# Optimization experiments

Hardware: AMD Instinct MI355X
Metric: run time of the kernel (lower is better)

## Reference

```python
import jax, jax.numpy as jnp
import numpy as np

B = 64          # batch_size
N_PER = 1000    # num_nodes per graph
NTOT = B * N_PER
H = 64          # hidden_gnn_dim


def _gcn_aggregate(x, senders, receivers, add_self_edges):
    """jraph.GraphConvolution aggregation with symmetric normalization.
    x: [NTOT, F] node features AFTER update_node_fn."""
    if add_self_edges:
        self_idx = jnp.arange(NTOT, dtype=senders.dtype)
        s = jnp.concatenate([senders, self_idx])
        r = jnp.concatenate([receivers, self_idx])
    else:
        s, r = senders, receivers
    ones = jnp.ones_like(s, dtype=x.dtype)
    deg_s = jax.ops.segment_sum(ones, s, num_segments=NTOT)
    deg_r = jax.ops.segment_sum(ones, r, num_segments=NTOT)
    x = x * jax.lax.rsqrt(jnp.maximum(deg_s, 1.0))[:, None]
    x = jax.ops.segment_sum(x[s], r, num_segments=NTOT)
    x = x * jax.lax.rsqrt(jnp.maximum(deg_r, 1.0))[:, None]
    return x


def setup_inputs() -> dict:
    key = jax.random.key(0)
    ks = jax.random.split(key, 12)
    n_edges = 1_000_000
    in_dim, fc, lat, out_dim = 64, 512, 64, 32
    flat = N_PER * H  # 64000

    def w(k, shape, fan_in):
        return jax.random.normal(k, shape, dtype=jnp.float32) / np.sqrt(fan_in)

    return {
        "nodes": jax.random.normal(ks[0], (NTOT, in_dim), dtype=jnp.float32),
        "senders": jax.random.randint(ks[1], (n_edges,), 0, NTOT),
        "receivers": jax.random.randint(ks[2], (n_edges,), 0, NTOT),
        "eps": jax.random.normal(ks[3], (B, lat), dtype=jnp.float32),
        "W_gcn1": w(ks[4], (in_dim, H), in_dim),
        "b_gcn1": jnp.zeros((H,), jnp.float32),
        "W_fc": w(ks[5], (flat, fc), flat),
        "b_fc": jnp.zeros((fc,), jnp.float32),
        "W_mean": w(ks[6], (fc, lat), fc),
        "b_mean": jnp.zeros((lat,), jnp.float32),
        "W_logstd": w(ks[7], (fc, lat), fc),
        "b_logstd": jnp.zeros((lat,), jnp.float32),
        "W_dec_fc": w(ks[8], (lat, flat), lat),
        "b_dec_fc": jnp.zeros((flat,), jnp.float32),
        "W_dec_out": w(ks[9], (H, out_dim), H),
        "b_dec_out": jnp.zeros((out_dim,), jnp.float32),
    }


def reference(nodes, senders, receivers, eps, W_gcn1, b_gcn1, W_fc, b_fc,
              W_mean, b_mean, W_logstd, b_logstd, W_dec_fc, b_dec_fc,
              W_dec_out, b_dec_out):
    # --- Encoder: GCN(update=Linear+relu, add_self_edges=True) ---
    h = jax.nn.relu(nodes @ W_gcn1 + b_gcn1)                 # [NTOT, H]
    h = _gcn_aggregate(h, senders, receivers, add_self_edges=True)
    x = h.reshape(B, N_PER * H)                              # flatten per graph
    x = jax.nn.relu(x @ W_fc + b_fc)                         # [B, fc]
    mean = x @ W_mean + b_mean                               # [B, lat]
    log_std = x @ W_logstd + b_logstd                        # [B, lat]
    # --- Reparameterization ---
    z = mean + jnp.exp(log_std) * eps                        # [B, lat]
    # --- Decoder ---
    d = jax.nn.relu(z @ W_dec_fc + b_dec_fc)                 # [B, N_PER*H]
    d = d.reshape(NTOT, H)
    d = d @ W_dec_out + b_dec_out                            # update_node_fn
    out_nodes = _gcn_aggregate(d, senders, receivers, add_self_edges=False)
    return mean, log_std, out_nodes
```

## Files before the change

kernel.cpp:

```cpp
#include <hip/hip_runtime.h>
#include <math.h>

#define NTOT 64000
#define HD   64
#define NB   64
#define FC   512
#define LAT  64
#define OUTD 32
#define GKC  128
#define NKB  500
#define NBH  128
#define NBUK 250
#define BSH  8
#define BCH  3968

typedef __bf16 bf16x8 __attribute__((ext_vector_type(8)));
typedef float  f32x4  __attribute__((ext_vector_type(4)));

__device__ inline float bflo(unsigned u) { union {unsigned q; float f;} x; x.q = u << 16; return x.f; }
__device__ inline float bfhi(unsigned u) { union {unsigned q; float f;} x; x.q = u & 0xFFFF0000u; return x.f; }
__device__ inline unsigned pkbf(float lo, float hi) {
  __bf16 a = (__bf16)lo, b = (__bf16)hi;
  unsigned short ua, ub;
  __builtin_memcpy(&ua, &a, 2); __builtin_memcpy(&ub, &b, 2);
  return (unsigned)ua | ((unsigned)ub << 16);
}

__global__ __launch_bounds__(256) void k_hist(const int* __restrict__ s,
    const int* __restrict__ r, unsigned* __restrict__ partials, int nE) {
  __shared__ unsigned hist[16000];
  int arr = blockIdx.y;
  const int* idx = arr ? r : s;
  unsigned* base = partials + ((size_t)arr * NBH + blockIdx.x) * 16000;
  for (int u = threadIdx.x; u < 16000; u += 256) hist[u] = 0;
  __syncthreads();
  int chunk = (nE + NBH - 1) / NBH;
  int e0 = blockIdx.x * chunk;
  int e1 = min(e0 + chunk, nE);
  for (int e = e0 + threadIdx.x; e < e1; e += 256) {
    int i = idx[e];
    atomicAdd(&hist[i >> 2], 1u << ((i & 3) * 8));
  }
  __syncthreads();
  for (int u = threadIdx.x; u < 16000; u += 256) base[u] = hist[u];
}

__global__ __launch_bounds__(256) void k_scan1(const unsigned* __restrict__ partials,
    int* __restrict__ rs, int* __restrict__ bsums,
    int* __restrict__ dout, int* __restrict__ din) {
  __shared__ int sm[256];
  __shared__ unsigned bw[64];
  int t = threadIdx.x;
  int w0 = blockIdx.x * 64;
  if (t < 64) {
    unsigned a = 0, b = 0;
    for (int bk = 0; bk < NBH; bk++) a += partials[(size_t)bk * 16000 + w0 + t];
    for (int bk = 0; bk < NBH; bk++) b += partials[((size_t)NBH + bk) * 16000 + w0 + t];
    bw[t] = b;
    *reinterpret_cast<int4*>(dout + (size_t)(w0 + t) * 4) =
        make_int4(a & 255, (a >> 8) & 255, (a >> 16) & 255, a >> 24);
    *reinterpret_cast<int4*>(din + (size_t)(w0 + t) * 4) =
        make_int4(b & 255, (b >> 8) & 255, (b >> 16) & 255, b >> 24);
  }
  __syncthreads();
  int v = (int)((bw[t >> 2] >> ((t & 3) * 8)) & 255u);
  sm[t] = v;
  __syncthreads();
  for (int d = 1; d < 256; d <<= 1) {
    int x = (t >= d) ? sm[t - d] : 0;
    __syncthreads();
    sm[t] += x;
    __syncthreads();
  }
  rs[blockIdx.x * 256 + t] = sm[t] - v;
  if (t == 255) bsums[blockIdx.x] = sm[255];
}

__global__ void k_scan2(int* __restrict__ rs, int* __restrict__ gcur,
                        const int* __restrict__ bsums, int nE) {
  __shared__ int sm[256];
  int bid = blockIdx.x, t = threadIdx.x;
  sm[t] = (t < bid) ? bsums[t] : 0;
  __syncthreads();
  for (int d = 128; d > 0; d >>= 1) {
    if (t < d) sm[t] += sm[t + d];
    __syncthreads();
  }
  int i = bid * 256 + t;
  int v = rs[i] + sm[0];
  rs[i] = v;
  if ((i & 255) == 0) gcur[i >> 8] = v;
  if (bid == 0 && t == 0) rs[NTOT] = nE;
}

__global__ __launch_bounds__(256) void k_bucket(const int* __restrict__ s,
    const int* __restrict__ r, int* __restrict__ gcur,
    unsigned* __restrict__ ebuf, int nE) {
  __shared__ int cnt[NBUK];
  __shared__ int base[NBUK];
  __shared__ int rbuf[BCH];
  int tid = threadIdx.x;
  int chunk = (nE + gridDim.x - 1) / gridDim.x;
  int e0 = blockIdx.x * chunk;
  int e1 = min(e0 + chunk, nE);
  for (int u = tid; u < NBUK; u += 256) cnt[u] = 0;
  __syncthreads();
  for (int e = e0 + tid; e < e1; e += 256) {
    int rr = r[e];
    rbuf[e - e0] = rr;
    atomicAdd(&cnt[rr >> BSH], 1);
  }
  __syncthreads();
  for (int u = tid; u < NBUK; u += 256) {
    base[u] = atomicAdd(&gcur[u], cnt[u]);
    cnt[u] = 0;
  }
  __syncthreads();
  for (int e = e0 + tid; e < e1; e += 256) {
    int rr = rbuf[e - e0];
    int b = rr >> BSH;
    int off = atomicAdd(&cnt[b], 1);
    ebuf[base[b] + off] = ((unsigned)(rr & 255) << 16) | (unsigned)s[e];
  }
}

__global__ __launch_bounds__(256) void k_fill2(const unsigned* __restrict__ ebuf,
    const int* __restrict__ rs, int* __restrict__ csr) {
  __shared__ int cur[256];
  int b = blockIdx.x;
  int tid = threadIdx.x;
  int nbase = b << BSH;
  cur[tid] = rs[nbase + tid];
  __syncthreads();
  int e0 = rs[nbase];
  int e1 = rs[nbase + 256];
  for (int e = e0 + tid; e < e1; e += 256) {
    unsigned p = ebuf[e];
    int pos = atomicAdd(&cur[p >> 16], 1);
    csr[pos] = (int)(p & 0xFFFFu);
  }
}

__global__ __launch_bounds__(256) void k_node1(const float* __restrict__ nodes,
    const float* __restrict__ W1, const float* __restrict__ b1,
    const int* __restrict__ dout, __bf16* __restrict__ h1) {
  __shared__ float wsm[HD * HD];
  int tid = threadIdx.x;
  for (int u = tid; u < HD * HD; u += 256) wsm[u] = W1[u];
  __syncthreads();
  int f = tid & 63, g = tid >> 6;
#pragma unroll
  for (int it = 0; it < 4; it++) {
    int node = blockIdx.x * 16 + it * 4 + g;
    const float* xr = nodes + (size_t)node * HD;
    float acc = b1[f];
#pragma unroll 16
    for (int k = 0; k < HD; k++) acc = fmaf(xr[k], wsm[k * HD + f], acc);
    acc = fmaxf(acc, 0.f);
    h1[(size_t)node * HD + f] = (__bf16)(acc * rsqrtf((float)(dout[node] + 1)));
  }
}

__global__ __launch_bounds__(256) void k_agg1(const unsigned* __restrict__ h1u,
    const int* __restrict__ rs, const int* __restrict__ csr,
    const int* __restrict__ din, unsigned* __restrict__ xbo) {
  int tid = threadIdx.x;
  int node = blockIdx.x * 8 + (tid >> 5);
  int f2 = tid & 31;
  int beg = rs[node], end = rs[node + 1];
  unsigned su = h1u[(size_t)node * 32 + f2];
  float a0 = bflo(su), b0 = bfhi(su);
  float a1 = 0, b1 = 0, a2 = 0, b2 = 0, a3 = 0, b3 = 0;
  float a4 = 0, b4 = 0, a5 = 0, b5 = 0, a6 = 0, b6 = 0, a7 = 0, b7 = 0;
  int e = beg;
  for (; e + 8 <= end; e += 8) {
    unsigned u0 = h1u[(size_t)csr[e] * 32 + f2];
    unsigned u1 = h1u[(size_t)csr[e + 1] * 32 + f2];
    unsigned u2 = h1u[(size_t)csr[e + 2] * 32 + f2];
    unsigned u3 = h1u[(size_t)csr[e + 3] * 32 + f2];
    unsigned u4 = h1u[(size_t)csr[e + 4] * 32 + f2];
    unsigned u5 = h1u[(size_t)csr[e + 5] * 32 + f2];
    unsigned u6 = h1u[(size_t)csr[e + 6] * 32 + f2];
    unsigned u7 = h1u[(size_t)csr[e + 7] * 32 + f2];
    a0 += bflo(u0); b0 += bfhi(u0);
    a1 += bflo(u1); b1 += bfhi(u1);
    a2 += bflo(u2); b2 += bfhi(u2);
    a3 += bflo(u3); b3 += bfhi(u3);
    a4 += bflo(u4); b4 += bfhi(u4);
    a5 += bflo(u5); b5 += bfhi(u5);
    a6 += bflo(u6); b6 += bfhi(u6);
    a7 += bflo(u7); b7 += bfhi(u7);
  }
  for (; e + 4 <= end; e += 4) {
    unsigned u0 = h1u[(size_t)csr[e] * 32 + f2];
    unsigned u1 = h1u[(size_t)csr[e + 1] * 32 + f2];
    unsigned u2 = h1u[(size_t)csr[e + 2] * 32 + f2];
    unsigned u3 = h1u[(size_t)csr[e + 3] * 32 + f2];
    a0 += bflo(u0); b0 += bfhi(u0);
    a1 += bflo(u1); b1 += bfhi(u1);
    a2 += bflo(u2); b2 += bfhi(u2);
    a3 += bflo(u3); b3 += bfhi(u3);
  }
  for (; e < end; e++) {
    unsigned u = h1u[(size_t)csr[e] * 32 + f2];
    a1 += bflo(u); b1 += bfhi(u);
  }
  float sc = rsqrtf((float)(din[node] + 1));
  float sa = ((a0 + a1) + (a2 + a3)) + ((a4 + a5) + (a6 + a7));
  float sb = ((b0 + b1) + (b2 + b3)) + ((b4 + b5) + (b6 + b7));
  xbo[(size_t)node * 32 + f2] = pkbf(sa * sc, sb * sc);
}

__global__ __launch_bounds__(512) void k_gemm(const __bf16* __restrict__ xb,
    const float* __restrict__ Wfc, unsigned* __restrict__ part) {
  __shared__ __align__(16) __bf16 As[64 * 136];
  int kb = blockIdx.x;
  int k0 = kb * GKC;
  int tid = threadIdx.x;
  for (int u = tid; u < 64 * 16; u += 512) {
    int row = u >> 4, c = u & 15;
    const uint4* src = reinterpret_cast<const uint4*>(xb + (size_t)row * 64000 + k0);
    reinterpret_cast<uint4*>(&As[row * 136])[c] = src[c];
  }
  __syncthreads();
  int w = tid >> 6, lane = tid & 63;
  int cw = lane & 15, kg = lane >> 4;
  const float* Bp = Wfc + ((size_t)k0 + kg * 8) * FC + w * 64 + cw;
  f32x4 acc[4][4];
#pragma unroll
  for (int mt = 0; mt < 4; mt++)
#pragma unroll
    for (int nt = 0; nt < 4; nt++) acc[mt][nt] = (f32x4){0.f, 0.f, 0.f, 0.f};

  for (int ks = 0; ks < 4; ks++) {
    bf16x8 bfrag[4];
#pragma unroll
    for (int nt = 0; nt < 4; nt++) {
      const float* bp = Bp + (size_t)ks * 32 * FC + nt * 16;
      bf16x8 bb;
#pragma unroll
      for (int b = 0; b < 8; b++) bb[b] = (__bf16)bp[(size_t)b * FC];
      bfrag[nt] = bb;
    }
    bf16x8 afrag[4];
#pragma unroll
    for (int mt = 0; mt < 4; mt++)
      afrag[mt] = *reinterpret_cast<const bf16x8*>(
          &As[(mt * 16 + cw) * 136 + ks * 32 + kg * 8]);
#pragma unroll
    for (int mt = 0; mt < 4; mt++)
#pragma unroll
      for (int nt = 0; nt < 4; nt++)
        acc[mt][nt] = __builtin_amdgcn_mfma_f32_16x16x32_bf16(
            afrag[mt], bfrag[nt], acc[mt][nt], 0, 0, 0);
  }
#pragma unroll
  for (int mt = 0; mt < 4; mt++)
#pragma unroll
    for (int nt = 0; nt < 4; nt++) {
      int col = w * 64 + nt * 16 + cw;
      size_t base = (size_t)kb * (FC * 32) + (size_t)col * 32 + mt * 8 + kg * 2;
      part[base]     = pkbf(acc[mt][nt][0], acc[mt][nt][1]);
      part[base + 1] = pkbf(acc[mt][nt][2], acc[mt][nt][3]);
    }
}

__global__ __launch_bounds__(256) void k_reduce(const unsigned* __restrict__ part,
    const float* __restrict__ bfc, float* __restrict__ xf) {
  __shared__ float slo[8][33];
  __shared__ float shi[8][33];
  int t = threadIdx.x;
  int pl = t & 31, sl = t >> 5;
  int c = blockIdx.x;
  size_t off = (size_t)c * 32 + pl;
  float lo0 = 0, hi0 = 0, lo1 = 0, hi1 = 0;
  int kb = sl;
  for (; kb + 16 < NKB; kb += 16) {
    unsigned u0 = part[(size_t)kb * (FC * 32) + off];
    unsigned u1 = part[(size_t)(kb + 8) * (FC * 32) + off];
    lo0 += bflo(u0); hi0 += bfhi(u0);
    lo1 += bflo(u1); hi1 += bfhi(u1);
  }
  for (; kb < NKB; kb += 8) {
    unsigned u0 = part[(size_t)kb * (FC * 32) + off];
    lo0 += bflo(u0); hi0 += bfhi(u0);
  }
  slo[sl][pl] = lo0 + lo1;
  shi[sl][pl] = hi0 + hi1;
  __syncthreads();
  if (t < 32) {
    float lo = 0, hi = 0;
#pragma unroll
    for (int s = 0; s < 8; s++) { lo += slo[s][t]; hi += shi[s][t]; }
    float bias = bfc[c];
    xf[(size_t)(2 * t) * FC + c]     = fmaxf(lo + bias, 0.f);
    xf[(size_t)(2 * t + 1) * FC + c] = fmaxf(hi + bias, 0.f);
  }
}

__global__ __launch_bounds__(256) void k_head(const float* __restrict__ xf,
    const float* __restrict__ Wm, const float* __restrict__ bm,
    const float* __restrict__ Wl, const float* __restrict__ bl,
    const float* __restrict__ eps, float* __restrict__ out_mean,
    float* __restrict__ out_logstd, float* __restrict__ z) {
  __shared__ float xr[FC];
  __shared__ float ps[4][LAT];
  __shared__ float zm[LAT];
  int b = blockIdx.x, t = threadIdx.x;
  for (int u = t; u < FC; u += 256) xr[u] = xf[b * FC + u];
  __syncthreads();
  int g = t >> 6;
  int l = t & 63;
  int h = g & 1;
  const float* W = (g < 2) ? Wm : Wl;
  float acc = 0.f;
  int kb = h * (FC / 2);
#pragma unroll 8
  for (int k = kb; k < kb + FC / 2; k++) acc = fmaf(xr[k], W[k * LAT + l], acc);
  ps[g][l] = acc;
  __syncthreads();
  float ls = 0.f;
  if (g == 0) {
    float m = ps[0][l] + ps[1][l] + bm[l];
    out_mean[b * 64 + l] = m;
    zm[l] = m;
  }
  if (g == 2) {
    ls = ps[2][l] + ps[3][l] + bl[l];
    out_logstd[b * 64 + l] = ls;
  }
  __syncthreads();
  if (g == 2) z[b * 64 + l] = zm[l] + expf(ls) * eps[b * 64 + l];
}

__global__ __launch_bounds__(256) void k_dec(const float* __restrict__ z,
    const float* __restrict__ Wdf, const float* __restrict__ bdf,
    const float* __restrict__ Wdo, const float* __restrict__ bdo,
    const int* __restrict__ deg, __bf16* __restrict__ dds) {
  __shared__ float zs[64 * 64];
  __shared__ float ws[64 * 65];
  __shared__ float ps[64 * 65];
  __shared__ float wo[64 * 32];
  int np = blockIdx.x, tid = threadIdx.x;
  for (int u = tid; u < 4096; u += 256) zs[u] = z[u];
  for (int u = tid; u < 4096; u += 256)
    ws[(u >> 6) * 65 + (u & 63)] = Wdf[(size_t)(u >> 6) * 64000 + np * 64 + (u & 63)];
  for (int u = tid; u < 2048; u += 256) wo[u] = Wdo[u];
  __syncthreads();
  {
    int h = tid & 63, bg = tid >> 6;
    float bias = bdf[np * 64 + h];
#pragma unroll
    for (int bb = 0; bb < 16; bb++) {
      int b = bg * 16 + bb;
      float acc = bias;
#pragma unroll 8
      for (int k = 0; k < 64; k++) acc = fmaf(zs[b * 64 + k], ws[k * 65 + h], acc);
      ps[b * 65 + h] = fmaxf(acc, 0.f);
    }
  }
  __syncthreads();
  {
    int o = tid & 31, bg = tid >> 5;
    float bias = bdo[o];
#pragma unroll
    for (int bb = 0; bb < 8; bb++) {
      int b = bg * 8 + bb;
      float acc = bias;
#pragma unroll 8
      for (int h = 0; h < 64; h++) acc = fmaf(ps[b * 65 + h], wo[h * 32 + o], acc);
      int node = b * 1000 + np;
      dds[(size_t)node * OUTD + o] =
          (__bf16)(acc * rsqrtf(fmaxf((float)deg[node], 1.f)));
    }
  }
}

__global__ __launch_bounds__(256) void k_agg2(const unsigned* __restrict__ ddsu,
    const int* __restrict__ rs, const int* __restrict__ csr,
    const int* __restrict__ din, float* __restrict__ outn) {
  int tid = threadIdx.x;
  int node = blockIdx.x * 16 + (tid >> 4);
  int f2 = tid & 15;
  int beg = rs[node], end = rs[node + 1];
  float a0 = 0, b0 = 0, a1 = 0, b1 = 0, a2 = 0, b2 = 0, a3 = 0, b3 = 0;
  float a4 = 0, b4 = 0, a5 = 0, b5 = 0, a6 = 0, b6 = 0, a7 = 0, b7 = 0;
  int e = beg;
  for (; e + 8 <= end; e += 8) {
    unsigned u0 = ddsu[(size_t)csr[e] * 16 + f2];
    unsigned u1 = ddsu[(size_t)csr[e + 1] * 16 + f2];
    unsigned u2 = ddsu[(size_t)csr[e + 2] * 16 + f2];
    unsigned u3 = ddsu[(size_t)csr[e + 3] * 16 + f2];
    unsigned u4 = ddsu[(size_t)csr[e + 4] * 16 + f2];
    unsigned u5 = ddsu[(size_t)csr[e + 5] * 16 + f2];
    unsigned u6 = ddsu[(size_t)csr[e + 6] * 16 + f2];
    unsigned u7 = ddsu[(size_t)csr[e + 7] * 16 + f2];
    a0 += bflo(u0); b0 += bfhi(u0);
    a1 += bflo(u1); b1 += bfhi(u1);
    a2 += bflo(u2); b2 += bfhi(u2);
    a3 += bflo(u3); b3 += bfhi(u3);
    a4 += bflo(u4); b4 += bfhi(u4);
    a5 += bflo(u5); b5 += bfhi(u5);
    a6 += bflo(u6); b6 += bfhi(u6);
    a7 += bflo(u7); b7 += bfhi(u7);
  }
  for (; e + 4 <= end; e += 4) {
    unsigned u0 = ddsu[(size_t)csr[e] * 16 + f2];
    unsigned u1 = ddsu[(size_t)csr[e + 1] * 16 + f2];
    unsigned u2 = ddsu[(size_t)csr[e + 2] * 16 + f2];
    unsigned u3 = ddsu[(size_t)csr[e + 3] * 16 + f2];
    a0 += bflo(u0); b0 += bfhi(u0);
    a1 += bflo(u1); b1 += bfhi(u1);
    a2 += bflo(u2); b2 += bfhi(u2);
    a3 += bflo(u3); b3 += bfhi(u3);
  }
  for (; e < end; e++) {
    unsigned u = ddsu[(size_t)csr[e] * 16 + f2];
    a1 += bflo(u); b1 += bfhi(u);
  }
  float sc = rsqrtf(fmaxf((float)din[node], 1.f));
  float sa = ((a0 + a1) + (a2 + a3)) + ((a4 + a5) + (a6 + a7));
  float sb = ((b0 + b1) + (b2 + b3)) + ((b4 + b5) + (b6 + b7));
  *reinterpret_cast<float2*>(outn + (size_t)node * 32 + f2 * 2) =
      make_float2(sa * sc, sb * sc);
}

extern "C" void kernel_launch(void* const* d_in, const int* in_sizes, int n_in,
                              void* d_out, int out_size, void* d_ws, size_t ws_size,
                              hipStream_t stream) {
  const float* nodes   = (const float*)d_in[0];
  const int*   senders = (const int*)d_in[1];
  const int*   recvs   = (const int*)d_in[2];
  const float* eps     = (const float*)d_in[3];
  const float* W1      = (const float*)d_in[4];
  const float* b1      = (const float*)d_in[5];
  const float* Wfc     = (const float*)d_in[6];
  const float* bfc     = (const float*)d_in[7];
  const float* Wm      = (const float*)d_in[8];
  const float* bm      = (const float*)d_in[9];
  const float* Wl      = (const float*)d_in[10];
  const float* bl      = (const float*)d_in[11];
  const float* Wdf     = (const float*)d_in[12];
  const float* bdf     = (const float*)d_in[13];
  const float* Wdo     = (const float*)d_in[14];
  const float* bdo     = (const float*)d_in[15];
  int nE = in_sizes[1];

  char* w = (char*)d_ws;
  auto alloc = [&](size_t bytes) {
    char* p = w;
    w += (bytes + 255) & ~(size_t)255;
    return p;
  };
  int* deg_out   = (int*)alloc((size_t)NTOT * 4);
  int* deg_in    = (int*)alloc((size_t)NTOT * 4);
  int* row_start = (int*)alloc((size_t)(NTOT + 1) * 4);
  int* gcur      = (int*)alloc((size_t)NBUK * 4);
  int* bsums     = (int*)alloc(256 * 4);
  int* csr       = (int*)alloc((size_t)nE * 4);
  unsigned* ebuf = (unsigned*)alloc((size_t)nE * 4);
  __bf16* h1  = (__bf16*)alloc((size_t)NTOT * HD * 2);
  __bf16* xb  = (__bf16*)alloc((size_t)NTOT * HD * 2);
  unsigned* part = (unsigned*)alloc((size_t)NKB * FC * 32 * 4);
  float* xf   = (float*)alloc((size_t)NB * FC * 4);
  float* z    = (float*)alloc((size_t)NB * LAT * 4);
  __bf16* dds  = xb;
  unsigned* partials = (unsigned*)part;

  float* out_mean   = (float*)d_out;
  float* out_logstd = (float*)d_out + 4096;
  float* out_nodes  = (float*)d_out + 8192;

  k_hist<<<dim3(NBH, 2), 256, 0, stream>>>(senders, recvs, partials, nE);
  k_scan1<<<NTOT / 256, 256, 0, stream>>>(partials, row_start, bsums, deg_out, deg_in);
  k_scan2<<<NTOT / 256, 256, 0, stream>>>(row_start, gcur, bsums, nE);
  k_bucket<<<256, 256, 0, stream>>>(senders, recvs, gcur, ebuf, nE);
  k_fill2<<<NBUK, 256, 0, stream>>>(ebuf, row_start, csr);
  k_node1<<<NTOT / 16, 256, 0, stream>>>(nodes, W1, b1, deg_out, h1);
  k_agg1<<<NTOT / 8, 256, 0, stream>>>((const unsigned*)h1, row_start, csr, deg_in, (unsigned*)xb);
  k_gemm<<<NKB, 512, 0, stream>>>(xb, Wfc, part);
  k_reduce<<<FC, 256, 0, stream>>>(part, bfc, xf);
  k_head<<<NB, 256, 0, stream>>>(xf, Wm, bm, Wl, bl, eps, out_mean, out_logstd, z);
  k_dec<<<1000, 256, 0, stream>>>(z, Wdf, bdf, Wdo, bdo, deg_out, dds);
  k_agg2<<<NTOT / 16, 256, 0, stream>>>((const unsigned*)dds, row_start, csr, deg_in, out_nodes);
}
```

Measured before the change: 238.9 us.

## Fuse CSR fill into first aggregation, use 16-bit CSR, parallelize scan1 reduction

Drops the separate k_fill2 kernel. A new k_fagg1 kernel builds each 256-node bucket's CSR slice in shared memory, writes it out as 16-bit sender indices, and then aggregates the first GCN layer from that local copy. The second aggregation reads the 16-bit CSR, which halves its index traffic. k_scan1 now spreads the histogram reduction across all 256 threads instead of 64. The price is a much coarser launch (250 blocks of 1024 threads, 8 nodes per warp-group in sequence), which may lower occupancy and latency hiding. Any bucket with more than 6144 edges would silently drop edges.

```diff
diff --git a/kernel.cpp b/kernel.cpp
--- a/kernel.cpp
+++ b/kernel.cpp
@@ -13,6 +13,7 @@
 #define NBUK 250
 #define BSH  8
 #define BCH  3968
+#define LCSR 6144
 
 typedef __bf16 bf16x8 __attribute__((ext_vector_type(8)));
 typedef float  f32x4  __attribute__((ext_vector_type(4)));
@@ -49,13 +50,25 @@
     int* __restrict__ rs, int* __restrict__ bsums,
     int* __restrict__ dout, int* __restrict__ din) {
   __shared__ int sm[256];
+  __shared__ unsigned pa[4][64];
+  __shared__ unsigned pb[4][64];
   __shared__ unsigned bw[64];
   int t = threadIdx.x;
   int w0 = blockIdx.x * 64;
+  int wd = t & 63, q = t >> 6;
+  {
+    unsigned a = 0, b = 0;
+    for (int bk = q * 32; bk < q * 32 + 32; bk++) {
+      a += partials[(size_t)bk * 16000 + w0 + wd];
+      b += partials[((size_t)NBH + bk) * 16000 + w0 + wd];
+    }
+    pa[q][wd] = a;
+    pb[q][wd] = b;
+  }
+  __syncthreads();
   if (t < 64) {
-    unsigned a = 0, b = 0;
-    for (int bk = 0; bk < NBH; bk++) a += partials[(size_t)bk * 16000 + w0 + t];
-    for (int bk = 0; bk < NBH; bk++) b += partials[((size_t)NBH + bk) * 16000 + w0 + t];
+    unsigned a = (pa[0][t] + pa[1][t]) + (pa[2][t] + pa[3][t]);
+    unsigned b = (pb[0][t] + pb[1][t]) + (pb[2][t] + pb[3][t]);
     bw[t] = b;
     *reinterpret_cast<int4*>(dout + (size_t)(w0 + t) * 4) =
         make_int4(a & 255, (a >> 8) & 255, (a >> 16) & 255, a >> 24);
@@ -124,23 +137,6 @@
   }
 }
 
-__global__ __launch_bounds__(256) void k_fill2(const unsigned* __restrict__ ebuf,
-    const int* __restrict__ rs, int* __restrict__ csr) {
-  __shared__ int cur[256];
-  int b = blockIdx.x;
-  int tid = threadIdx.x;
-  int nbase = b << BSH;
-  cur[tid] = rs[nbase + tid];
-  __syncthreads();
-  int e0 = rs[nbase];
-  int e1 = rs[nbase + 256];
-  for (int e = e0 + tid; e < e1; e += 256) {
-    unsigned p = ebuf[e];
-    int pos = atomicAdd(&cur[p >> 16], 1);
-    csr[pos] = (int)(p & 0xFFFFu);
-  }
-}
-
 __global__ __launch_bounds__(256) void k_node1(const float* __restrict__ nodes,
     const float* __restrict__ W1, const float* __restrict__ b1,
     const int* __restrict__ dout, __bf16* __restrict__ h1) {
@@ -161,54 +157,75 @@
   }
 }
 
-__global__ __launch_bounds__(256) void k_agg1(const unsigned* __restrict__ h1u,
-    const int* __restrict__ rs, const int* __restrict__ csr,
-    const int* __restrict__ din, unsigned* __restrict__ xbo) {
-  int tid = threadIdx.x;
-  int node = blockIdx.x * 8 + (tid >> 5);
-  int f2 = tid & 31;
-  int beg = rs[node], end = rs[node + 1];
-  unsigned su = h1u[(size_t)node * 32 + f2];
-  float a0 = bflo(su), b0 = bfhi(su);
-  float a1 = 0, b1 = 0, a2 = 0, b2 = 0, a3 = 0, b3 = 0;
-  float a4 = 0, b4 = 0, a5 = 0, b5 = 0, a6 = 0, b6 = 0, a7 = 0, b7 = 0;
-  int e = beg;
-  for (; e + 8 <= end; e += 8) {
-    unsigned u0 = h1u[(size_t)csr[e] * 32 + f2];
-    unsigned u1 = h1u[(size_t)csr[e + 1] * 32 + f2];
-    unsigned u2 = h1u[(size_t)csr[e + 2] * 32 + f2];
-    unsigned u3 = h1u[(size_t)csr[e + 3] * 32 + f2];
-    unsigned u4 = h1u[(size_t)csr[e + 4] * 32 + f2];
-    unsigned u5 = h1u[(size_t)csr[e + 5] * 32 + f2];
-    unsigned u6 = h1u[(size_t)csr[e + 6] * 32 + f2];
-    unsigned u7 = h1u[(size_t)csr[e + 7] * 32 + f2];
-    a0 += bflo(u0); b0 += bfhi(u0);
-    a1 += bflo(u1); b1 += bfhi(u1);
-    a2 += bflo(u2); b2 += bfhi(u2);
-    a3 += bflo(u3); b3 += bfhi(u3);
-    a4 += bflo(u4); b4 += bfhi(u4);
-    a5 += bflo(u5); b5 += bfhi(u5);
-    a6 += bflo(u6); b6 += bfhi(u6);
-    a7 += bflo(u7); b7 += bfhi(u7);
-  }
-  for (; e + 4 <= end; e += 4) {
-    unsigned u0 = h1u[(size_t)csr[e] * 32 + f2];
-    unsigned u1 = h1u[(size_t)csr[e + 1] * 32 + f2];
-    unsigned u2 = h1u[(size_t)csr[e + 2] * 32 + f2];
-    unsigned u3 = h1u[(size_t)csr[e + 3] * 32 + f2];
-    a0 += bflo(u0); b0 += bfhi(u0);
-    a1 += bflo(u1); b1 += bfhi(u1);
-    a2 += bflo(u2); b2 += bfhi(u2);
-    a3 += bflo(u3); b3 += bfhi(u3);
-  }
-  for (; e < end; e++) {
-    unsigned u = h1u[(size_t)csr[e] * 32 + f2];
-    a1 += bflo(u); b1 += bfhi(u);
-  }
-  float sc = rsqrtf((float)(din[node] + 1));
-  float sa = ((a0 + a1) + (a2 + a3)) + ((a4 + a5) + (a6 + a7));
-  float sb = ((b0 + b1) + (b2 + b3)) + ((b4 + b5) + (b6 + b7));
-  xbo[(size_t)node * 32 + f2] = pkbf(sa * sc, sb * sc);
+__global__ __launch_bounds__(1024) void k_fagg1(const unsigned* __restrict__ h1u,
+    const unsigned* __restrict__ ebuf, const int* __restrict__ rs,
+    const int* __restrict__ din, unsigned* __restrict__ xbo,
+    unsigned short* __restrict__ csr16) {
+  __shared__ unsigned short lcsr[LCSR];
+  __shared__ int cur[256];
+  int b = blockIdx.x, tid = threadIdx.x;
+  int nbase = b << BSH;
+  int e0 = rs[nbase];
+  int e1 = rs[nbase + 256];
+  int ne = e1 - e0;
+  if (tid < 256) cur[tid] = rs[nbase + tid] - e0;
+  __syncthreads();
+  for (int e = tid; e < ne; e += 1024) {
+    unsigned p = ebuf[e0 + e];
+    int pos = atomicAdd(&cur[p >> 16], 1);
+    if (pos < LCSR) lcsr[pos] = (unsigned short)(p & 0xFFFFu);
+  }
+  __syncthreads();
+  for (int e = tid; e < ne; e += 1024) csr16[e0 + e] = lcsr[e];
+  int grp = tid >> 5, f2 = tid & 31;
+#pragma unroll
+  for (int ni = 0; ni < 8; ni++) {
+    int n = grp * 8 + ni;
+    int node = nbase + n;
+    int end = cur[n];
+    int beg = (n == 0) ? 0 : cur[n - 1];
+    unsigned su = h1u[(size_t)node * 32 + f2];
+    float a0 = bflo(su), b0 = bfhi(su);
+    float a1 = 0, b1 = 0, a2 = 0, b2 = 0, a3 = 0, b3 = 0;
+    float a4 = 0, b4 = 0, a5 = 0, b5 = 0, a6 = 0, b6 = 0, a7 = 0, b7 = 0;
+    int e = beg;
+    for (; e + 8 <= end; e += 8) {
+      unsigned u0 = h1u[(size_t)lcsr[e] * 32 + f2];
+      unsigned u1 = h1u[(size_t)lcsr[e + 1] * 32 + f2];
+      unsigned u2 = h1u[(size_t)lcsr[e + 2] * 32 + f2];
+      unsigned u3 = h1u[(size_t)lcsr[e + 3] * 32 + f2];
+      unsigned u4 = h1u[(size_t)lcsr[e + 4] * 32 + f2];
+      unsigned u5 = h1u[(size_t)lcsr[e + 5] * 32 + f2];
+      unsigned u6 = h1u[(size_t)lcsr[e + 6] * 32 + f2];
+      unsigned u7 = h1u[(size_t)lcsr[e + 7] * 32 + f2];
+      a0 += bflo(u0); b0 += bfhi(u0);
+      a1 += bflo(u1); b1 += bfhi(u1);
+      a2 += bflo(u2); b2 += bfhi(u2);
+      a3 += bflo(u3); b3 += bfhi(u3);
+      a4 += bflo(u4); b4 += bfhi(u4);
+      a5 += bflo(u5); b5 += bfhi(u5);
+      a6 += bflo(u6); b6 += bfhi(u6);
+      a7 += bflo(u7); b7 += bfhi(u7);
+    }
+    for (; e + 4 <= end; e += 4) {
+      unsigned u0 = h1u[(size_t)lcsr[e] * 32 + f2];
+      unsigned u1 = h1u[(size_t)lcsr[e + 1] * 32 + f2];
+      unsigned u2 = h1u[(size_t)lcsr[e + 2] * 32 + f2];
+      unsigned u3 = h1u[(size_t)lcsr[e + 3] * 32 + f2];
+      a0 += bflo(u0); b0 += bfhi(u0);
+      a1 += bflo(u1); b1 += bfhi(u1);
+      a2 += bflo(u2); b2 += bfhi(u2);
+      a3 += bflo(u3); b3 += bfhi(u3);
+    }
+    for (; e < end; e++) {
+      unsigned u = h1u[(size_t)lcsr[e] * 32 + f2];
+      a1 += bflo(u); b1 += bfhi(u);
+    }
+    float sc = rsqrtf((float)(din[node] + 1));
+    float sa = ((a0 + a1) + (a2 + a3)) + ((a4 + a5) + (a6 + a7));
+    float sb = ((b0 + b1) + (b2 + b3)) + ((b4 + b5) + (b6 + b7));
+    xbo[(size_t)node * 32 + f2] = pkbf(sa * sc, sb * sc);
+  }
 }
 
 __global__ __launch_bounds__(512) void k_gemm(const __bf16* __restrict__ xb,
@@ -377,7 +394,7 @@
 }
 
 __global__ __launch_bounds__(256) void k_agg2(const unsigned* __restrict__ ddsu,
-    const int* __restrict__ rs, const int* __restrict__ csr,
+    const int* __restrict__ rs, const unsigned short* __restrict__ csr16,
     const int* __restrict__ din, float* __restrict__ outn) {
   int tid = threadIdx.x;
   int node = blockIdx.x * 16 + (tid >> 4);
@@ -387,14 +404,14 @@
   float a4 = 0, b4 = 0, a5 = 0, b5 = 0, a6 = 0, b6 = 0, a7 = 0, b7 = 0;
   int e = beg;
   for (; e + 8 <= end; e += 8) {
-    unsigned u0 = ddsu[(size_t)csr[e] * 16 + f2];
-    unsigned u1 = ddsu[(size_t)csr[e + 1] * 16 + f2];
-    unsigned u2 = ddsu[(size_t)csr[e + 2] * 16 + f2];
-    unsigned u3 = ddsu[(size_t)csr[e + 3] * 16 + f2];
-    unsigned u4 = ddsu[(size_t)csr[e + 4] * 16 + f2];
-    unsigned u5 = ddsu[(size_t)csr[e + 5] * 16 + f2];
-    unsigned u6 = ddsu[(size_t)csr[e + 6] * 16 + f2];
-    unsigned u7 = ddsu[(size_t)csr[e + 7] * 16 + f2];
+    unsigned u0 = ddsu[(size_t)csr16[e] * 16 + f2];
+    unsigned u1 = ddsu[(size_t)csr16[e + 1] * 16 + f2];
+    unsigned u2 = ddsu[(size_t)csr16[e + 2] * 16 + f2];
+    unsigned u3 = ddsu[(size_t)csr16[e + 3] * 16 + f2];
+    unsigned u4 = ddsu[(size_t)csr16[e + 4] * 16 + f2];
+    unsigned u5 = ddsu[(size_t)csr16[e + 5] * 16 + f2];
+    unsigned u6 = ddsu[(size_t)csr16[e + 6] * 16 + f2];
+    unsigned u7 = ddsu[(size_t)csr16[e + 7] * 16 + f2];
     a0 += bflo(u0); b0 += bfhi(u0);
     a1 += bflo(u1); b1 += bfhi(u1);
     a2 += bflo(u2); b2 += bfhi(u2);
@@ -405,17 +422,17 @@
     a7 += bflo(u7); b7 += bfhi(u7);
   }
   for (; e + 4 <= end; e += 4) {
-    unsigned u0 = ddsu[(size_t)csr[e] * 16 + f2];
-    unsigned u1 = ddsu[(size_t)csr[e + 1] * 16 + f2];
-    unsigned u2 = ddsu[(size_t)csr[e + 2] * 16 + f2];
-    unsigned u3 = ddsu[(size_t)csr[e + 3] * 16 + f2];
+    unsigned u0 = ddsu[(size_t)csr16[e] * 16 + f2];
+    unsigned u1 = ddsu[(size_t)csr16[e + 1] * 16 + f2];
+    unsigned u2 = ddsu[(size_t)csr16[e + 2] * 16 + f2];
+    unsigned u3 = ddsu[(size_t)csr16[e + 3] * 16 + f2];
     a0 += bflo(u0); b0 += bfhi(u0);
     a1 += bflo(u1); b1 += bfhi(u1);
     a2 += bflo(u2); b2 += bfhi(u2);
     a3 += bflo(u3); b3 += bfhi(u3);
   }
   for (; e < end; e++) {
-    unsigned u = ddsu[(size_t)csr[e] * 16 + f2];
+    unsigned u = ddsu[(size_t)csr16[e] * 16 + f2];
     a1 += bflo(u); b1 += bfhi(u);
   }
   float sc = rsqrtf(fmaxf((float)din[node], 1.f));
@@ -457,7 +474,7 @@
   int* row_start = (int*)alloc((size_t)(NTOT + 1) * 4);
   int* gcur      = (int*)alloc((size_t)NBUK * 4);
   int* bsums     = (int*)alloc(256 * 4);
-  int* csr       = (int*)alloc((size_t)nE * 4);
+  unsigned short* csr16 = (unsigned short*)alloc((size_t)nE * 2);
   unsigned* ebuf = (unsigned*)alloc((size_t)nE * 4);
   __bf16* h1  = (__bf16*)alloc((size_t)NTOT * HD * 2);
   __bf16* xb  = (__bf16*)alloc((size_t)NTOT * HD * 2);
@@ -475,12 +492,12 @@
   k_scan1<<<NTOT / 256, 256, 0, stream>>>(partials, row_start, bsums, deg_out, deg_in);
   k_scan2<<<NTOT / 256, 256, 0, stream>>>(row_start, gcur, bsums, nE);
   k_bucket<<<256, 256, 0, stream>>>(senders, recvs, gcur, ebuf, nE);
-  k_fill2<<<NBUK, 256, 0, stream>>>(ebuf, row_start, csr);
   k_node1<<<NTOT / 16, 256, 0, stream>>>(nodes, W1, b1, deg_out, h1);
-  k_agg1<<<NTOT / 8, 256, 0, stream>>>((const unsigned*)h1, row_start, csr, deg_in, (unsigned*)xb);
+  k_fagg1<<<NBUK, 1024, 0, stream>>>((const unsigned*)h1, ebuf, row_start, deg_in,
+                                     (unsigned*)xb, csr16);
   k_gemm<<<NKB, 512, 0, stream>>>(xb, Wfc, part);
   k_reduce<<<FC, 256, 0, stream>>>(part, bfc, xf);
   k_head<<<NB, 256, 0, stream>>>(xf, Wm, bm, Wl, bl, eps, out_mean, out_logstd, z);
   k_dec<<<1000, 256, 0, stream>>>(z, Wdf, bdf, Wdo, bdo, deg_out, dds);
-  k_agg2<<<NTOT / 16, 256, 0, stream>>>((const unsigned*)dds, row_start, csr, deg_in, out_nodes);
-}
+  k_agg2<<<NTOT / 16, 256, 0, stream>>>((const unsigned*)dds, row_start, csr16, deg_in, out_nodes);
+}
```

Measured after the change: 222.2 us, median of 2. 7.0% less time.
